# Kernel optimization log

Hardware: AMD Instinct MI355X
Metric: run time of the kernel (lower is better)

## Reference

```python
import jax, jax.numpy as jnp
import numpy as np

N = 50000   # nodes
E = 800000  # edges before self-loops
H = 4       # heads
D = 64      # num_h_feats (per-head out dim of hidden layers)
C = 2       # num_classes
NEG = 0.2   # DGL GATConv leaky_relu negative_slope
EPS = 1e-5  # BatchNorm eps


def setup_inputs() -> dict:
    key = jax.random.key(0)
    ks = jax.random.split(key, 16)
    inp = {}
    inp['feats'] = jax.random.normal(ks[0], (N, 9), jnp.float32)
    inp['W1'] = jax.random.normal(ks[1], (9, H * D), jnp.float32) * 0.1
    inp['al1'] = jax.random.normal(ks[2], (H, D), jnp.float32) * 0.1
    inp['ar1'] = jax.random.normal(ks[3], (H, D), jnp.float32) * 0.1
    inp['b1'] = jnp.zeros((H, D), jnp.float32)
    inp['Wm'] = jax.random.normal(ks[4], (D, H * D), jnp.float32) * 0.1
    inp['alm'] = jax.random.normal(ks[5], (H, D), jnp.float32) * 0.1
    inp['arm'] = jax.random.normal(ks[6], (H, D), jnp.float32) * 0.1
    inp['bm'] = jnp.zeros((H, D), jnp.float32)
    inp['W2'] = jax.random.normal(ks[7], (D, H * C), jnp.float32) * 0.1
    inp['al2'] = jax.random.normal(ks[8], (H, C), jnp.float32) * 0.1
    inp['ar2'] = jax.random.normal(ks[9], (H, C), jnp.float32) * 0.1
    inp['b2'] = jnp.zeros((H, C), jnp.float32)
    inp['gamma'] = jnp.ones((D,), jnp.float32)
    inp['beta'] = jnp.zeros((D,), jnp.float32)
    inp['src'] = jax.random.randint(ks[10], (E,), 0, N, jnp.int32)
    inp['dst'] = jax.random.randint(ks[11], (E,), 0, N, jnp.int32)
    return inp


def gat_layer(x, W, al, ar, b, src, dst, out_d):
    """DGL GATConv: linear -> per-edge attention -> dst-softmax -> scatter-sum."""
    n = x.shape[0]
    z = (x @ W).reshape(n, H, out_d)                 # [N, H, Dout]
    el = jnp.sum(z * al, axis=-1)                    # [N, H] attn on src
    er = jnp.sum(z * ar, axis=-1)                    # [N, H] attn on dst
    e = jax.nn.leaky_relu(el[src] + er[dst], NEG)    # [E, H]
    m = jax.ops.segment_max(e, dst, num_segments=n)  # per-dst max (stable softmax)
    a = jnp.exp(e - m[dst])
    s = jax.ops.segment_sum(a, dst, num_segments=n)
    alpha = a / s[dst]                               # [E, H]
    out = jax.ops.segment_sum(alpha[:, :, None] * z[src], dst, num_segments=n)
    return out + b                                   # [N, H, Dout]


def batchnorm(h, gamma, beta):
    mu = jnp.mean(h, axis=0)
    var = jnp.var(h, axis=0)
    return (h - mu) * jax.lax.rsqrt(var + EPS) * gamma + beta


def reference(feats, W1, al1, ar1, b1, Wm, alm, arm, bm, W2, al2, ar2, b2,
              gamma, beta, src, dst):
    # dgl.add_self_loop
    loop = jnp.arange(N, dtype=src.dtype)
    s = jnp.concatenate([src, loop])
    d = jnp.concatenate([dst, loop])
    h = gat_layer(feats, W1, al1, ar1, b1, s, d, D).sum(axis=1)  # head-sum
    h = batchnorm(h, gamma, beta)
    h = gat_layer(h, Wm, alm, arm, bm, s, d, D).sum(axis=1)
    h = batchnorm(h, gamma, beta)
    o = gat_layer(h, W2, al2, ar2, b2, s, d, C).sum(axis=1)      # [N, C]
    return o
```

## Files before the change

kernel.cpp:

```cpp
#include <hip/hip_runtime.h>
#include <hip/hip_bf16.h>

typedef __hip_bfloat16 bf16;
typedef __bf16 bf16x8 __attribute__((ext_vector_type(8)));
typedef float f32x4 __attribute__((ext_vector_type(4)));
typedef _Float16 h16;
typedef _Float16 h16x4 __attribute__((ext_vector_type(4)));

__device__ __forceinline__ float b2f(bf16 v) { return __bfloat162float(v); }

__device__ __forceinline__ float ldin(const void* p, size_t i, int isb) {
    return isb ? b2f(((const bf16*)p)[i]) : ((const float*)p)[i];
}
__device__ __forceinline__ unsigned short f2bfbits(float f) {
    bf16 v = __float2bfloat16(f);
    return *(unsigned short*)&v;
}

__global__ __launch_bounds__(256) void prep_kernel(
    const void* __restrict__ feats, const void* __restrict__ W1, const void* __restrict__ Wm,
    const void* __restrict__ al1, const void* __restrict__ ar1,
    const void* __restrict__ alm, const void* __restrict__ arm,
    const unsigned* __restrict__ gbits,
    unsigned short* __restrict__ fpad, unsigned short* __restrict__ W1T,
    unsigned short* __restrict__ WmT,
    float* __restrict__ alf1, float* __restrict__ arf1,
    float* __restrict__ alfm, float* __restrict__ arfm,
    int* __restrict__ flag, int Nn) {
    int isb = (gbits[0] == 0x3F803F80u) ? 1 : 0;
    long t = (long)blockIdx.x * 256 + threadIdx.x;
    if (t == 0) *flag = isb;
    long n64 = (long)Nn * 64;
    if (t < n64) {
        int k = (int)(t & 63); long n = t >> 6;
        fpad[t] = (k < 9) ? f2bfbits(ldin(feats, (size_t)n * 9 + k, isb)) : 0;
    } else if (t < n64 + 16384) {
        long u = t - n64; int n = (int)(u >> 6), k = (int)(u & 63);
        W1T[u] = (k < 9) ? f2bfbits(ldin(W1, (size_t)k * 256 + n, isb)) : 0;
    } else if (t < n64 + 32768) {
        long u = t - n64 - 16384; int n = (int)(u >> 6), k = (int)(u & 63);
        WmT[u] = f2bfbits(ldin(Wm, (size_t)k * 256 + n, isb));
    } else if (t < n64 + 32768 + 256) {
        int u = (int)(t - n64 - 32768);
        alf1[u] = ldin(al1, u, isb); arf1[u] = ldin(ar1, u, isb);
        alfm[u] = ldin(alm, u, isb); arfm[u] = ldin(arm, u, isb);
    }
}

__global__ __launch_bounds__(256) void count_kernel(
    const int* __restrict__ dst, int* __restrict__ deg, int E) {
    int t = blockIdx.x * 256 + threadIdx.x;
    if (t < E) atomicAdd(&deg[dst[t]], 1);
}

__global__ __launch_bounds__(256) void scan1_kernel(
    const int* __restrict__ deg, int* __restrict__ off, int* __restrict__ bsum, int Nn) {
    __shared__ int s[256];
    int t = threadIdx.x, i = blockIdx.x * 256 + t;
    int v = (i < Nn) ? deg[i] : 0;
    s[t] = v; __syncthreads();
#pragma unroll
    for (int o = 1; o < 256; o <<= 1) {
        int a = (t >= o) ? s[t - o] : 0;
        __syncthreads();
        s[t] += a;
        __syncthreads();
    }
    if (i < Nn) off[i] = s[t];
    if (t == 255) bsum[blockIdx.x] = s[255];
}

__global__ __launch_bounds__(256) void scan2_kernel(int* __restrict__ bsum, int NB) {
    __shared__ int s[256];
    int t = threadIdx.x;
    int v = (t < NB) ? bsum[t] : 0;
    s[t] = v; __syncthreads();
#pragma unroll
    for (int o = 1; o < 256; o <<= 1) {
        int a = (t >= o) ? s[t - o] : 0;
        __syncthreads();
        s[t] += a;
        __syncthreads();
    }
    if (t < NB) bsum[t] = s[t] - v;
}

__global__ __launch_bounds__(256) void scan3_kernel(
    const int* __restrict__ deg, int* __restrict__ off, int* __restrict__ cur,
    const int* __restrict__ bsum, int Nn, int E) {
    int i = blockIdx.x * 256 + threadIdx.x;
    if (i < Nn) {
        int ex = off[i] - deg[i] + bsum[i >> 8];
        off[i] = ex;
        cur[i] = ex;
    }
    if (i == 0) off[Nn] = E;
}

__global__ __launch_bounds__(256) void scatter_kernel(
    const int* __restrict__ src, const int* __restrict__ dst,
    int* __restrict__ cur, int* __restrict__ adj, int E) {
    int t = blockIdx.x * 256 + threadIdx.x;
    if (t < E) {
        int p = atomicAdd(&cur[dst[t]], 1);
        adj[p] = src[t];
    }
}


__global__ __launch_bounds__(256) void lin_mfma_l1_kernel(
    const unsigned short* __restrict__ xb, const unsigned short* __restrict__ WT,
    const float* __restrict__ alf, const float* __restrict__ arf,
    h16* __restrict__ zh, float* __restrict__ el, float* __restrict__ er, int Nn) {
    __shared__ h16 zs[16 * 256];
    int w = threadIdx.x >> 6;
    int l = threadIdx.x & 63;
    int quad = l >> 4, lc = l & 15;
    int node0 = blockIdx.x * 16;

    int mrow = node0 + lc; if (mrow >= Nn) mrow = Nn - 1;
    const bf16x8* xa = (const bf16x8*)(xb + (size_t)mrow * 64);
    bf16x8 a0 = xa[quad];
    bf16x8 a1 = xa[quad + 4];

    float pe[4] = {0.f, 0.f, 0.f, 0.f}, pr[4] = {0.f, 0.f, 0.f, 0.f};
    int row0 = quad * 4;
#pragma unroll
    for (int ct = 0; ct < 4; ++ct) {
        int col = w * 64 + ct * 16 + lc;
        const bf16x8* wb = (const bf16x8*)(WT + (size_t)col * 64);
        bf16x8 b0 = wb[quad];
        bf16x8 b1 = wb[quad + 4];
        f32x4 c = {0.f, 0.f, 0.f, 0.f};
        c = __builtin_amdgcn_mfma_f32_16x16x32_bf16(a0, b0, c, 0, 0, 0);
        c = __builtin_amdgcn_mfma_f32_16x16x32_bf16(a1, b1, c, 0, 0, 0);
        float av = alf[col], rv = arf[col];
#pragma unroll
        for (int r = 0; r < 4; ++r) {
            pe[r] = fmaf(c[r], av, pe[r]);
            pr[r] = fmaf(c[r], rv, pr[r]);
            zs[(row0 + r) * 256 + col] = (h16)c[r];
        }
    }
#pragma unroll
    for (int o = 1; o < 16; o <<= 1) {
#pragma unroll
        for (int r = 0; r < 4; ++r) {
            pe[r] += __shfl_xor(pe[r], o);
            pr[r] += __shfl_xor(pr[r], o);
        }
    }
    if (lc == 0) {
#pragma unroll
        for (int r = 0; r < 4; ++r) {
            int n = node0 + row0 + r;
            if (n < Nn) { el[n * 4 + w] = pe[r]; er[n * 4 + w] = pr[r]; }
        }
    }
    __syncthreads();
#pragma unroll
    for (int it = 0; it < 2; ++it) {
        int flat = it * 2048 + threadIdx.x * 8;
        int row = flat >> 8;
        if (node0 + row < Nn)
            *(uint4*)(zh + (size_t)node0 * 256 + flat) = *(const uint4*)(zs + flat);
    }
}

__global__ __launch_bounds__(256) void lin_mfma_bn_kernel(
    const float* __restrict__ x, const float* __restrict__ sc, const float* __restrict__ shb,
    const unsigned short* __restrict__ WT,
    const float* __restrict__ alf, const float* __restrict__ arf,
    h16* __restrict__ zh, float* __restrict__ el, float* __restrict__ er, int Nn) {
    __shared__ h16 zs[16 * 256];
    int w = threadIdx.x >> 6;
    int l = threadIdx.x & 63;
    int quad = l >> 4, lc = l & 15;
    int node0 = blockIdx.x * 16;

    int mrow = node0 + lc; if (mrow >= Nn) mrow = Nn - 1;
    const float* xr = x + (size_t)mrow * 64 + quad * 8;
    float4 f0 = ((const float4*)xr)[0];
    float4 f1 = ((const float4*)xr)[1];
    float4 f2 = ((const float4*)(xr + 32))[0];
    float4 f3 = ((const float4*)(xr + 32))[1];
    float4 s0 = ((const float4*)(sc + quad * 8))[0];
    float4 s1 = ((const float4*)(sc + quad * 8))[1];
    float4 s2 = ((const float4*)(sc + 32 + quad * 8))[0];
    float4 s3 = ((const float4*)(sc + 32 + quad * 8))[1];
    float4 h0 = ((const float4*)(shb + quad * 8))[0];
    float4 h1 = ((const float4*)(shb + quad * 8))[1];
    float4 h2 = ((const float4*)(shb + 32 + quad * 8))[0];
    float4 h3 = ((const float4*)(shb + 32 + quad * 8))[1];

    union { bf16x8 v; unsigned short s[8]; } ua, ub;
    ua.s[0] = f2bfbits(fmaf(f0.x, s0.x, h0.x));
    ua.s[1] = f2bfbits(fmaf(f0.y, s0.y, h0.y));
    ua.s[2] = f2bfbits(fmaf(f0.z, s0.z, h0.z));
    ua.s[3] = f2bfbits(fmaf(f0.w, s0.w, h0.w));
    ua.s[4] = f2bfbits(fmaf(f1.x, s1.x, h1.x));
    ua.s[5] = f2bfbits(fmaf(f1.y, s1.y, h1.y));
    ua.s[6] = f2bfbits(fmaf(f1.z, s1.z, h1.z));
    ua.s[7] = f2bfbits(fmaf(f1.w, s1.w, h1.w));
    ub.s[0] = f2bfbits(fmaf(f2.x, s2.x, h2.x));
    ub.s[1] = f2bfbits(fmaf(f2.y, s2.y, h2.y));
    ub.s[2] = f2bfbits(fmaf(f2.z, s2.z, h2.z));
    ub.s[3] = f2bfbits(fmaf(f2.w, s2.w, h2.w));
    ub.s[4] = f2bfbits(fmaf(f3.x, s3.x, h3.x));
    ub.s[5] = f2bfbits(fmaf(f3.y, s3.y, h3.y));
    ub.s[6] = f2bfbits(fmaf(f3.z, s3.z, h3.z));
    ub.s[7] = f2bfbits(fmaf(f3.w, s3.w, h3.w));
    bf16x8 a0 = ua.v, a1 = ub.v;

    float pe[4] = {0.f, 0.f, 0.f, 0.f}, pr[4] = {0.f, 0.f, 0.f, 0.f};
    int row0 = quad * 4;
#pragma unroll
    for (int ct = 0; ct < 4; ++ct) {
        int col = w * 64 + ct * 16 + lc;
        const bf16x8* wb = (const bf16x8*)(WT + (size_t)col * 64);
        bf16x8 b0 = wb[quad];
        bf16x8 b1 = wb[quad + 4];
        f32x4 c = {0.f, 0.f, 0.f, 0.f};
        c = __builtin_amdgcn_mfma_f32_16x16x32_bf16(a0, b0, c, 0, 0, 0);
        c = __builtin_amdgcn_mfma_f32_16x16x32_bf16(a1, b1, c, 0, 0, 0);
        float av = alf[col], rv = arf[col];
#pragma unroll
        for (int r = 0; r < 4; ++r) {
            pe[r] = fmaf(c[r], av, pe[r]);
            pr[r] = fmaf(c[r], rv, pr[r]);
            zs[(row0 + r) * 256 + col] = (h16)c[r];
        }
    }
#pragma unroll
    for (int o = 1; o < 16; o <<= 1) {
#pragma unroll
        for (int r = 0; r < 4; ++r) {
            pe[r] += __shfl_xor(pe[r], o);
            pr[r] += __shfl_xor(pr[r], o);
        }
    }
    if (lc == 0) {
#pragma unroll
        for (int r = 0; r < 4; ++r) {
            int n = node0 + row0 + r;
            if (n < Nn) { el[n * 4 + w] = pe[r]; er[n * 4 + w] = pr[r]; }
        }
    }
    __syncthreads();
#pragma unroll
    for (int it = 0; it < 2; ++it) {
        int flat = it * 2048 + threadIdx.x * 8;
        int row = flat >> 8;
        if (node0 + row < Nn)
            *(uint4*)(zh + (size_t)node0 * 256 + flat) = *(const uint4*)(zs + flat);
    }
}

__global__ void bn_coef_kernel(
    const float* __restrict__ bnsum, const float* __restrict__ bnsumsq,
    const void* __restrict__ gamma, const void* __restrict__ beta,
    float* __restrict__ sc, float* __restrict__ shb,
    const int* __restrict__ flag, int Nn) {
    int isb = *flag;
    int d = threadIdx.x;
    if (d >= 64) return;
    float inv_n = 1.f / (float)Nn;
    float mu = bnsum[d] * inv_n;
    float var = bnsumsq[d] * inv_n - mu * mu;
    float s = rsqrtf(var + 1e-5f) * ldin(gamma, d, isb);
    sc[d] = s;
    shb[d] = ldin(beta, d, isb) - mu * s;
}

__global__ __launch_bounds__(256) void lin3_kernel(
    const float* __restrict__ x, const float* __restrict__ sc, const float* __restrict__ shb,
    const void* __restrict__ W, const void* __restrict__ al, const void* __restrict__ ar,
    float* __restrict__ zc, float* __restrict__ el, float* __restrict__ er,
    const int* __restrict__ flag, int Nn) {
    int isb = *flag;
    int t = blockIdx.x * 256 + threadIdx.x;
    if (t >= Nn * 4) return;
    int n = t >> 2, h = t & 3;
    const float* xr = x + (size_t)n * 64;
    float a0 = 0.f, a1 = 0.f;
#pragma unroll 8
    for (int k = 0; k < 64; k++) {
        float xn = fmaf(xr[k], sc[k], shb[k]);
        a0 += xn * ldin(W, k * 8 + h * 2 + 0, isb);
        a1 += xn * ldin(W, k * 8 + h * 2 + 1, isb);
    }
    zc[n * 8 + h * 2 + 0] = a0;
    zc[n * 8 + h * 2 + 1] = a1;
    el[t] = a0 * ldin(al, h * 2, isb) + a1 * ldin(al, h * 2 + 1, isb);
    er[t] = a0 * ldin(ar, h * 2, isb) + a1 * ldin(ar, h * 2 + 1, isb);
}

__global__ __launch_bounds__(256) void gat_agg64_kernel(
    const h16* __restrict__ zh, const float* __restrict__ el, const float* __restrict__ er,
    const int* __restrict__ off, const int* __restrict__ adj, const void* __restrict__ bias,
    float* __restrict__ x, float* __restrict__ bnsum, float* __restrict__ bnsumsq,
    const int* __restrict__ flag, int Nn, int total_waves) {
    __shared__ __align__(16) float s_sum[4][64], s_sq[4][64];
    int isb = *flag;
    int tid = threadIdx.x;
    int wv = tid >> 6;
    int l = tid & 63;
    int h = l >> 4, q = l & 15;
    int gw = blockIdx.x * 4 + wv;

    float4 bsl;
    bsl.x = ldin(bias, h * 64 + q * 4 + 0, isb);
    bsl.y = ldin(bias, h * 64 + q * 4 + 1, isb);
    bsl.z = ldin(bias, h * 64 + q * 4 + 2, isb);
    bsl.w = ldin(bias, h * 64 + q * 4 + 3, isb);

    float4 bs = {0.f, 0.f, 0.f, 0.f}, bq = {0.f, 0.f, 0.f, 0.f};

    for (int n = gw; n < Nn; n += total_waves) {
        float er_nh = er[n * 4 + h];
        float e0 = el[n * 4 + h] + er_nh;
        e0 = (e0 > 0.f) ? e0 : 0.2f * e0;
        float w0 = __expf(e0);
        h16x4 zsh = ((const h16x4*)(zh + (size_t)n * 256))[h * 16 + q];
        float4 acc;
        acc.x = w0 * (float)zsh.x; acc.y = w0 * (float)zsh.y;
        acc.z = w0 * (float)zsh.z; acc.w = w0 * (float)zsh.w;
        float lsum = w0;
        int s0 = off[n], s1 = off[n + 1];
        for (int i = s0; i < s1; i += 8) {
            int ss[8];
#pragma unroll
            for (int j = 0; j < 8; j++) {
                int idx = i + j;
                ss[j] = adj[idx < s1 ? idx : s1 - 1];
            }
            float ev[8];
#pragma unroll
            for (int j = 0; j < 8; j++) ev[j] = el[ss[j] * 4 + h];
            h16x4 zv[8];
#pragma unroll
            for (int j = 0; j < 8; j++)
                zv[j] = ((const h16x4*)(zh + (size_t)ss[j] * 256))[h * 16 + q];
#pragma unroll
            for (int j = 0; j < 8; j++) {
                float e = ev[j] + er_nh;
                e = (e > 0.f) ? e : 0.2f * e;
                float w = __expf(e);
                if (i + j >= s1) w = 0.f;
                lsum += w;
                acc.x = fmaf(w, (float)zv[j].x, acc.x);
                acc.y = fmaf(w, (float)zv[j].y, acc.y);
                acc.z = fmaf(w, (float)zv[j].z, acc.z);
                acc.w = fmaf(w, (float)zv[j].w, acc.w);
            }
        }
        float inv = 1.f / lsum;
        float4 r;
        r.x = fmaf(acc.x, inv, bsl.x);
        r.y = fmaf(acc.y, inv, bsl.y);
        r.z = fmaf(acc.z, inv, bsl.z);
        r.w = fmaf(acc.w, inv, bsl.w);
#pragma unroll
        for (int o = 16; o < 64; o <<= 1) {
            r.x += __shfl_xor(r.x, o);
            r.y += __shfl_xor(r.y, o);
            r.z += __shfl_xor(r.z, o);
            r.w += __shfl_xor(r.w, o);
        }
        if (h == 0) {
            ((float4*)(x + (size_t)n * 64))[q] = r;
            bs.x += r.x; bs.y += r.y; bs.z += r.z; bs.w += r.w;
            bq.x = fmaf(r.x, r.x, bq.x); bq.y = fmaf(r.y, r.y, bq.y);
            bq.z = fmaf(r.z, r.z, bq.z); bq.w = fmaf(r.w, r.w, bq.w);
        }
    }
    if (h == 0) {
        ((float4*)&s_sum[wv][0])[q] = bs;
        ((float4*)&s_sq[wv][0])[q] = bq;
    }
    __syncthreads();
    if (tid < 64) {
        float s = s_sum[0][tid] + s_sum[1][tid] + s_sum[2][tid] + s_sum[3][tid];
        float qq = s_sq[0][tid] + s_sq[1][tid] + s_sq[2][tid] + s_sq[3][tid];
        atomicAdd(&bnsum[tid], s);
        atomicAdd(&bnsumsq[tid], qq);
    }
}

__global__ __launch_bounds__(256) void gat_agg2_kernel(
    const float* __restrict__ zc, const float* __restrict__ el, const float* __restrict__ er,
    const int* __restrict__ off, const int* __restrict__ adj, const void* __restrict__ bias,
    void* __restrict__ out, const int* __restrict__ flag, int Nn) {
    int isb = *flag;
    int t = blockIdx.x * 256 + threadIdx.x;
    if (t >= Nn * 4) return;
    int n = t >> 2, h = t & 3;
    float er_nh = er[n * 4 + h];
    float e0 = el[n * 4 + h] + er_nh;
    e0 = (e0 > 0.f) ? e0 : 0.2f * e0;
    float w0 = __expf(e0);
    float lsum = w0;
    float2 zn = ((const float2*)zc)[n * 4 + h];
    float a0 = w0 * zn.x, a1 = w0 * zn.y;
    int s0 = off[n], s1 = off[n + 1];
    for (int i = s0; i < s1; i += 4) {
        int ss[4];
#pragma unroll
        for (int j = 0; j < 4; j++) {
            int idx = i + j; if (idx >= s1) idx = s1 - 1;
            ss[j] = adj[idx];
        }
        float ev[4]; float2 zj[4];
#pragma unroll
        for (int j = 0; j < 4; j++) {
            ev[j] = el[ss[j] * 4 + h];
            zj[j] = ((const float2*)zc)[ss[j] * 4 + h];
        }
#pragma unroll
        for (int j = 0; j < 4; j++) {
            float e = ev[j] + er_nh;
            e = (e > 0.f) ? e : 0.2f * e;
            float w = __expf(e);
            if (i + j >= s1) w = 0.f;
            lsum += w;
            a0 = fmaf(w, zj[j].x, a0);
            a1 = fmaf(w, zj[j].y, a1);
        }
    }
    float inv = 1.f / lsum;
    float v0 = fmaf(a0, inv, ldin(bias, h * 2 + 0, isb));
    float v1 = fmaf(a1, inv, ldin(bias, h * 2 + 1, isb));
#pragma unroll
    for (int o = 1; o < 4; o <<= 1) {
        v0 += __shfl_xor(v0, o);
        v1 += __shfl_xor(v1, o);
    }
    if (h == 0) {
        if (isb) {
            ((bf16*)out)[n * 2 + 0] = __float2bfloat16(v0);
            ((bf16*)out)[n * 2 + 1] = __float2bfloat16(v1);
        } else {
            ((float*)out)[n * 2 + 0] = v0;
            ((float*)out)[n * 2 + 1] = v1;
        }
    }
}

extern "C" void kernel_launch(void* const* d_in, const int* in_sizes, int n_in,
                              void* d_out, int out_size, void* d_ws, size_t ws_size,
                              hipStream_t stream) {
    const void* feats = d_in[0];
    const void* W1    = d_in[1];
    const void* al1   = d_in[2];
    const void* ar1   = d_in[3];
    const void* b1    = d_in[4];
    const void* Wm    = d_in[5];
    const void* alm   = d_in[6];
    const void* arm   = d_in[7];
    const void* bm    = d_in[8];
    const void* W2    = d_in[9];
    const void* al2   = d_in[10];
    const void* ar2   = d_in[11];
    const void* b2v   = d_in[12];
    const void* gamma = d_in[13];
    const void* beta  = d_in[14];
    const int*  src   = (const int*)d_in[15];
    const int*  dst   = (const int*)d_in[16];

    int Nn = in_sizes[0] / 9;
    int E  = in_sizes[15];

    float* ws = (float*)d_ws;
    h16*   zh   = (h16*)ws;
    float* zc   = ws + (size_t)Nn * 128;
    float* el   = zc + (size_t)Nn * 8;
    float* er   = el + (size_t)Nn * 4;
    float* x    = er + (size_t)Nn * 4;
    float* bns1 = x + (size_t)Nn * 64;
    float* bnq1 = bns1 + 64;
    float* bns2 = bnq1 + 64;
    float* bnq2 = bns2 + 64;
    float* sc1  = bnq2 + 64;
    float* shb1 = sc1 + 64;
    float* sc2  = shb1 + 64;
    float* shb2 = sc2 + 64;
    float* alf1 = shb2 + 64;
    float* arf1 = alf1 + 256;
    float* alfm = arf1 + 256;
    float* arfm = alfm + 256;
    unsigned short* fpad = (unsigned short*)(arfm + 256);
    unsigned short* W1T  = fpad + (size_t)Nn * 64;
    unsigned short* WmT  = W1T + 256 * 64;
    int*   flag = (int*)(WmT + 256 * 64);
    int*   deg  = flag + 1;
    int*   off  = deg + Nn;
    int*   cur  = off + Nn + 1;
    int*   adj  = cur + Nn;
    int*   bsum = adj + E;

    dim3 B(256);
    int NB1 = (Nn + 255) / 256;
    int gE  = (E + 255) / 256;
    int gMF  = (Nn + 15) / 16;
    int gN4 = (Nn * 4 + 255) / 256;
    long prepN = (long)Nn * 64 + 32768 + 256;
    int gPrep = (int)((prepN + 255) / 256);
    int AGG_GRID = 2048;
    int total_waves = AGG_GRID * 4;

    prep_kernel<<<gPrep, B, 0, stream>>>(feats, W1, Wm, al1, ar1, alm, arm,
                                         (const unsigned*)gamma, fpad, W1T, WmT,
                                         alf1, arf1, alfm, arfm, flag, Nn);

    hipMemsetAsync(deg, 0, (size_t)Nn * sizeof(int), stream);
    hipMemsetAsync(bns1, 0, 256 * sizeof(float), stream);
    count_kernel<<<gE, B, 0, stream>>>(dst, deg, E);
    scan1_kernel<<<NB1, B, 0, stream>>>(deg, off, bsum, Nn);
    scan2_kernel<<<1, B, 0, stream>>>(bsum, NB1);
    scan3_kernel<<<NB1, B, 0, stream>>>(deg, off, cur, bsum, Nn, E);
    scatter_kernel<<<gE, B, 0, stream>>>(src, dst, cur, adj, E);

    lin_mfma_l1_kernel<<<gMF, B, 0, stream>>>(fpad, W1T, alf1, arf1, zh, el, er, Nn);
    gat_agg64_kernel<<<AGG_GRID, B, 0, stream>>>(zh, el, er, off, adj, b1, x, bns1, bnq1, flag, Nn, total_waves);
    bn_coef_kernel<<<1, 64, 0, stream>>>(bns1, bnq1, gamma, beta, sc1, shb1, flag, Nn);

    lin_mfma_bn_kernel<<<gMF, B, 0, stream>>>(x, sc1, shb1, WmT, alfm, arfm, zh, el, er, Nn);
    gat_agg64_kernel<<<AGG_GRID, B, 0, stream>>>(zh, el, er, off, adj, bm, x, bns2, bnq2, flag, Nn, total_waves);
    bn_coef_kernel<<<1, 64, 0, stream>>>(bns2, bnq2, gamma, beta, sc2, shb2, flag, Nn);

    lin3_kernel<<<gN4, B, 0, stream>>>(x, sc2, shb2, W2, al2, ar2, zc, el, er, flag, Nn);
    gat_agg2_kernel<<<gN4, B, 0, stream>>>(zc, el, er, off, adj, b2v, d_out, flag, Nn);
}
```

Measured before the change: 468.6 us.

## Merge graph-build and BN-coefficient kernels to cut launch count

Folds the degree-count into the prep kernel, and the scatter into the layer-1 linear kernel, by giving each launch extra block ranges. The two-pass block-sum scan becomes a per-block reduction of the preceding block sums. BN coefficient computation moves into the last-finishing aggregation block via an atomic counter, and the two memsets are merged into one. This removes about five launches and their serialization gaps, at the cost of redundant reduction work in the scan and a last-block fence pattern.

Result: slower. 531.3 us (+13.4%).

```diff
diff --git a/kernel.cpp b/kernel.cpp
--- a/kernel.cpp
+++ b/kernel.cpp
@@ -17,7 +17,7 @@
     return *(unsigned short*)&v;
 }
 
-__global__ __launch_bounds__(256) void prep_kernel(
+__global__ __launch_bounds__(256) void prep_count_kernel(
     const void* __restrict__ feats, const void* __restrict__ W1, const void* __restrict__ Wm,
     const void* __restrict__ al1, const void* __restrict__ ar1,
     const void* __restrict__ alm, const void* __restrict__ arm,
@@ -26,7 +26,14 @@
     unsigned short* __restrict__ WmT,
     float* __restrict__ alf1, float* __restrict__ arf1,
     float* __restrict__ alfm, float* __restrict__ arfm,
-    int* __restrict__ flag, int Nn) {
+    int* __restrict__ flag,
+    const int* __restrict__ dst, int* __restrict__ deg,
+    int Nn, int E, int gPrep) {
+    if ((int)blockIdx.x >= gPrep) {
+        int e = ((int)blockIdx.x - gPrep) * 256 + threadIdx.x;
+        if (e < E) atomicAdd(&deg[dst[e]], 1);
+        return;
+    }
     int isb = (gbits[0] == 0x3F803F80u) ? 1 : 0;
     long t = (long)blockIdx.x * 256 + threadIdx.x;
     if (t == 0) *flag = isb;
@@ -47,12 +54,6 @@
     }
 }
 
-__global__ __launch_bounds__(256) void count_kernel(
-    const int* __restrict__ dst, int* __restrict__ deg, int E) {
-    int t = blockIdx.x * 256 + threadIdx.x;
-    if (t < E) atomicAdd(&deg[dst[t]], 1);
-}
-
 __global__ __launch_bounds__(256) void scan1_kernel(
     const int* __restrict__ deg, int* __restrict__ off, int* __restrict__ bsum, int Nn) {
     __shared__ int s[256];
@@ -70,53 +71,49 @@
     if (t == 255) bsum[blockIdx.x] = s[255];
 }
 
-__global__ __launch_bounds__(256) void scan2_kernel(int* __restrict__ bsum, int NB) {
+__global__ __launch_bounds__(256) void scan3b_kernel(
+    const int* __restrict__ deg, int* __restrict__ off, int* __restrict__ cur,
+    const int* __restrict__ bsum, int Nn, int E, int NB) {
     __shared__ int s[256];
-    int t = threadIdx.x;
-    int v = (t < NB) ? bsum[t] : 0;
-    s[t] = v; __syncthreads();
-#pragma unroll
-    for (int o = 1; o < 256; o <<= 1) {
-        int a = (t >= o) ? s[t - o] : 0;
+    int b = blockIdx.x, t = threadIdx.x;
+    s[t] = (t < b && t < NB) ? bsum[t] : 0;
+    __syncthreads();
+#pragma unroll
+    for (int o = 128; o > 0; o >>= 1) {
+        if (t < o) s[t] += s[t + o];
         __syncthreads();
-        s[t] += a;
-        __syncthreads();
-    }
-    if (t < NB) bsum[t] = s[t] - v;
-}
-
-__global__ __launch_bounds__(256) void scan3_kernel(
-    const int* __restrict__ deg, int* __restrict__ off, int* __restrict__ cur,
-    const int* __restrict__ bsum, int Nn, int E) {
-    int i = blockIdx.x * 256 + threadIdx.x;
+    }
+    int base = s[0];
+    int i = b * 256 + t;
     if (i < Nn) {
-        int ex = off[i] - deg[i] + bsum[i >> 8];
+        int ex = off[i] - deg[i] + base;
         off[i] = ex;
         cur[i] = ex;
     }
     if (i == 0) off[Nn] = E;
 }
 
-__global__ __launch_bounds__(256) void scatter_kernel(
+__global__ __launch_bounds__(256) void scatter_lin1_kernel(
     const int* __restrict__ src, const int* __restrict__ dst,
-    int* __restrict__ cur, int* __restrict__ adj, int E) {
-    int t = blockIdx.x * 256 + threadIdx.x;
-    if (t < E) {
-        int p = atomicAdd(&cur[dst[t]], 1);
-        adj[p] = src[t];
-    }
-}
-
-
-__global__ __launch_bounds__(256) void lin_mfma_l1_kernel(
+    int* __restrict__ cur, int* __restrict__ adj, int E,
     const unsigned short* __restrict__ xb, const unsigned short* __restrict__ WT,
     const float* __restrict__ alf, const float* __restrict__ arf,
-    h16* __restrict__ zh, float* __restrict__ el, float* __restrict__ er, int Nn) {
+    h16* __restrict__ zh, float* __restrict__ el, float* __restrict__ er,
+    int Nn, int gE) {
     __shared__ h16 zs[16 * 256];
+    if ((int)blockIdx.x < gE) {
+        int t = (int)blockIdx.x * 256 + threadIdx.x;
+        if (t < E) {
+            int p = atomicAdd(&cur[dst[t]], 1);
+            adj[p] = src[t];
+        }
+        return;
+    }
+    int bid = (int)blockIdx.x - gE;
     int w = threadIdx.x >> 6;
     int l = threadIdx.x & 63;
     int quad = l >> 4, lc = l & 15;
-    int node0 = blockIdx.x * 16;
+    int node0 = bid * 16;
 
     int mrow = node0 + lc; if (mrow >= Nn) mrow = Nn - 1;
     const bf16x8* xa = (const bf16x8*)(xb + (size_t)mrow * 64);
@@ -256,22 +253,6 @@
     }
 }
 
-__global__ void bn_coef_kernel(
-    const float* __restrict__ bnsum, const float* __restrict__ bnsumsq,
-    const void* __restrict__ gamma, const void* __restrict__ beta,
-    float* __restrict__ sc, float* __restrict__ shb,
-    const int* __restrict__ flag, int Nn) {
-    int isb = *flag;
-    int d = threadIdx.x;
-    if (d >= 64) return;
-    float inv_n = 1.f / (float)Nn;
-    float mu = bnsum[d] * inv_n;
-    float var = bnsumsq[d] * inv_n - mu * mu;
-    float s = rsqrtf(var + 1e-5f) * ldin(gamma, d, isb);
-    sc[d] = s;
-    shb[d] = ldin(beta, d, isb) - mu * s;
-}
-
 __global__ __launch_bounds__(256) void lin3_kernel(
     const float* __restrict__ x, const float* __restrict__ sc, const float* __restrict__ shb,
     const void* __restrict__ W, const void* __restrict__ al, const void* __restrict__ ar,
@@ -299,8 +280,11 @@
     const h16* __restrict__ zh, const float* __restrict__ el, const float* __restrict__ er,
     const int* __restrict__ off, const int* __restrict__ adj, const void* __restrict__ bias,
     float* __restrict__ x, float* __restrict__ bnsum, float* __restrict__ bnsumsq,
+    const void* __restrict__ gamma, const void* __restrict__ beta,
+    float* __restrict__ sc, float* __restrict__ shb, int* __restrict__ ctr,
     const int* __restrict__ flag, int Nn, int total_waves) {
     __shared__ __align__(16) float s_sum[4][64], s_sq[4][64];
+    __shared__ int s_last;
     int isb = *flag;
     int tid = threadIdx.x;
     int wv = tid >> 6;
@@ -384,6 +368,23 @@
         float qq = s_sq[0][tid] + s_sq[1][tid] + s_sq[2][tid] + s_sq[3][tid];
         atomicAdd(&bnsum[tid], s);
         atomicAdd(&bnsumsq[tid], qq);
+    }
+    __syncthreads();
+    if (tid == 0) {
+        __threadfence();
+        int old = atomicAdd(ctr, 1);
+        s_last = (old == (int)gridDim.x - 1) ? 1 : 0;
+    }
+    __syncthreads();
+    if (s_last && tid < 64) {
+        float ssum = atomicAdd(&bnsum[tid], 0.0f);
+        float sqq  = atomicAdd(&bnsumsq[tid], 0.0f);
+        float inv_n = 1.f / (float)Nn;
+        float mu = ssum * inv_n;
+        float var = sqq * inv_n - mu * mu;
+        float s = rsqrtf(var + 1e-5f) * ldin(gamma, tid, isb);
+        sc[tid] = s;
+        shb[tid] = ldin(beta, tid, isb) - mu * s;
     }
 }
 
@@ -476,11 +477,15 @@
     float* el   = zc + (size_t)Nn * 8;
     float* er   = el + (size_t)Nn * 4;
     float* x    = er + (size_t)Nn * 4;
-    float* bns1 = x + (size_t)Nn * 64;
+    int*   deg  = (int*)(x + (size_t)Nn * 64);
+    float* bns1 = (float*)(deg + Nn);
     float* bnq1 = bns1 + 64;
     float* bns2 = bnq1 + 64;
     float* bnq2 = bns2 + 64;
-    float* sc1  = bnq2 + 64;
+    int*   ctr1 = (int*)(bnq2 + 64);
+    int*   ctr2 = ctr1 + 1;
+    size_t msetBytes = (size_t)Nn * 4 + 256 * 4 + 16;
+    float* sc1  = (float*)(ctr1 + 4);
     float* shb1 = sc1 + 64;
     float* sc2  = shb1 + 64;
     float* shb2 = sc2 + 64;
@@ -492,8 +497,7 @@
     unsigned short* W1T  = fpad + (size_t)Nn * 64;
     unsigned short* WmT  = W1T + 256 * 64;
     int*   flag = (int*)(WmT + 256 * 64);
-    int*   deg  = flag + 1;
-    int*   off  = deg + Nn;
+    int*   off  = flag + 1;
     int*   cur  = off + Nn + 1;
     int*   adj  = cur + Nn;
     int*   bsum = adj + E;
@@ -501,32 +505,33 @@
     dim3 B(256);
     int NB1 = (Nn + 255) / 256;
     int gE  = (E + 255) / 256;
-    int gMF  = (Nn + 15) / 16;
+    int gMF = (Nn + 15) / 16;
     int gN4 = (Nn * 4 + 255) / 256;
     long prepN = (long)Nn * 64 + 32768 + 256;
     int gPrep = (int)((prepN + 255) / 256);
     int AGG_GRID = 2048;
     int total_waves = AGG_GRID * 4;
 
-    prep_kernel<<<gPrep, B, 0, stream>>>(feats, W1, Wm, al1, ar1, alm, arm,
-                                         (const unsigned*)gamma, fpad, W1T, WmT,
-                                         alf1, arf1, alfm, arfm, flag, Nn);
-
-    hipMemsetAsync(deg, 0, (size_t)Nn * sizeof(int), stream);
-    hipMemsetAsync(bns1, 0, 256 * sizeof(float), stream);
-    count_kernel<<<gE, B, 0, stream>>>(dst, deg, E);
+    hipMemsetAsync(deg, 0, msetBytes, stream);
+
+    prep_count_kernel<<<gPrep + gE, B, 0, stream>>>(
+        feats, W1, Wm, al1, ar1, alm, arm, (const unsigned*)gamma,
+        fpad, W1T, WmT, alf1, arf1, alfm, arfm, flag, dst, deg, Nn, E, gPrep);
+
     scan1_kernel<<<NB1, B, 0, stream>>>(deg, off, bsum, Nn);
-    scan2_kernel<<<1, B, 0, stream>>>(bsum, NB1);
-    scan3_kernel<<<NB1, B, 0, stream>>>(deg, off, cur, bsum, Nn, E);
-    scatter_kernel<<<gE, B, 0, stream>>>(src, dst, cur, adj, E);
-
-    lin_mfma_l1_kernel<<<gMF, B, 0, stream>>>(fpad, W1T, alf1, arf1, zh, el, er, Nn);
-    gat_agg64_kernel<<<AGG_GRID, B, 0, stream>>>(zh, el, er, off, adj, b1, x, bns1, bnq1, flag, Nn, total_waves);
-    bn_coef_kernel<<<1, 64, 0, stream>>>(bns1, bnq1, gamma, beta, sc1, shb1, flag, Nn);
+    scan3b_kernel<<<NB1, B, 0, stream>>>(deg, off, cur, bsum, Nn, E, NB1);
+
+    scatter_lin1_kernel<<<gE + gMF, B, 0, stream>>>(
+        src, dst, cur, adj, E, fpad, W1T, alf1, arf1, zh, el, er, Nn, gE);
+
+    gat_agg64_kernel<<<AGG_GRID, B, 0, stream>>>(
+        zh, el, er, off, adj, b1, x, bns1, bnq1, gamma, beta, sc1, shb1, ctr1,
+        flag, Nn, total_waves);
 
     lin_mfma_bn_kernel<<<gMF, B, 0, stream>>>(x, sc1, shb1, WmT, alfm, arfm, zh, el, er, Nn);
-    gat_agg64_kernel<<<AGG_GRID, B, 0, stream>>>(zh, el, er, off, adj, bm, x, bns2, bnq2, flag, Nn, total_waves);
-    bn_coef_kernel<<<1, 64, 0, stream>>>(bns2, bnq2, gamma, beta, sc2, shb2, flag, Nn);
+    gat_agg64_kernel<<<AGG_GRID, B, 0, stream>>>(
+        zh, el, er, off, adj, bm, x, bns2, bnq2, gamma, beta, sc2, shb2, ctr2,
+        flag, Nn, total_waves);
 
     lin3_kernel<<<gN4, B, 0, stream>>>(x, sc2, shb2, W2, al2, ar2, zc, el, er, flag, Nn);
     gat_agg2_kernel<<<gN4, B, 0, stream>>>(zc, el, er, off, adj, b2v, d_out, flag, Nn);
```
